# Performance work log

Measured on AMD Instinct MI355X. Metric: run time of the kernel, lower is better.

Reference implementation:

```python
import jax, jax.numpy as jnp
import numpy as np

FS = 11        # filter_size
N_ITER = 5     # mean-field iterations


def _unfold(x, fs):
    """x: (B, C, Hp, Wp) padded -> patches (B, C, H, W, fs, fs) with
    patches[b,c,h,w,i,j] == x[b,c,h+i,w+j]."""
    B, C, Hp, Wp = x.shape
    H, W = Hp - fs + 1, Wp - fs + 1
    p = jax.lax.conv_general_dilated_patches(
        x.reshape(B * C, 1, Hp, Wp), (fs, fs), (1, 1), 'VALID')  # (B*C, fs*fs, H, W)
    return p.reshape(B, C, fs, fs, H, W).transpose(0, 1, 4, 5, 2, 3)


def _smoothing_filter(fs, inv_bw, spacings):
    """Gaussian spatial filter with zeroed center, shape (B, fs, fs)."""
    r = jnp.arange(-(fs // 2), fs // 2 + 1, dtype=spacings.dtype)
    d = jnp.stack(jnp.meshgrid(r, r, indexing='ij'))           # (2, fs, fs)
    d = d[None] * spacings[:, :, None, None]                   # (B, 2, fs, fs)
    f = jnp.exp(-jnp.sum((d * inv_bw) ** 2 / 2, axis=1))       # (B, fs, fs)
    return f.at[:, fs // 2, fs // 2].set(0.0)


def setup_inputs() -> dict:
    key = jax.random.key(0)
    k1, k2 = jax.random.split(key)
    B, C, CH, H, W = 2, 6, 3, 192, 192
    return {
        'x': jax.random.normal(k1, (B, C, H, W), dtype=jnp.float32),
        'features': jax.random.normal(k2, (B, CH, H, W), dtype=jnp.float32),
        'spatial_spacings': jnp.ones((B, 2), dtype=jnp.float32),
        'smoothing_weight': jnp.array(1.0, dtype=jnp.float32),
        'appearance_weight': jnp.array(1.0, dtype=jnp.float32),
        'inverse_smoothing_bandwidth': jnp.array(1.0, dtype=jnp.float32),
        'inverse_appearance_bandwidth': jnp.array(1.0, dtype=jnp.float32),
    }


def reference(x, features, spatial_spacings, smoothing_weight, appearance_weight,
              inverse_smoothing_bandwidth, inverse_appearance_bandwidth):
    fs, pad = FS, FS // 2
    B, C, H, W = x.shape
    pad_cfg = [(0, 0), (0, 0), (pad, pad), (pad, pad)]

    # Spatial Gaussian filter (iteration-independent).
    sf = _smoothing_filter(fs, inverse_smoothing_bandwidth, spatial_spacings)  # (B,fs,fs)

    # Bilateral (appearance) filter, also iteration-independent -> hoisted.
    fpatch = _unfold(jnp.pad(features, pad_cfg), fs)           # (B,ch,H,W,fs,fs)
    diffs = features[..., None, None] - fpatch
    af = jnp.exp(-jnp.sum((diffs * inverse_appearance_bandwidth) ** 2 / 2, axis=1))  # (B,H,W,fs,fs)
    af = af.at[..., fs // 2, fs // 2].set(0.0)

    # combined message filter: w_s * sf + w_a * sf * af  (center tap already zero)
    sfb = sf[:, None, None]                                    # (B,1,1,fs,fs)
    total_filter = smoothing_weight * jnp.broadcast_to(sfb, af.shape) + appearance_weight * sfb * af

    compat = -jnp.eye(C, dtype=x.dtype)                        # Potts compatibility mu(l,l') = -[l==l']
    negative_unary = x
    for _ in range(N_ITER):
        q = jax.nn.softmax(x, axis=1)
        qpatch = _unfold(jnp.pad(q, pad_cfg), fs)              # (B,C,H,W,fs,fs)
        msg = jnp.einsum('bhwij,bchwij->bchw', total_filter, qpatch)
        x = negative_unary - jnp.einsum('bjhw,jk->bkhw', msg, compat)
    return jax.nn.log_softmax(x, axis=1)
```

## Files before the change

kernel.cpp:

```cpp
#include <hip/hip_runtime.h>

#define HH 192
#define WW 192
#define BB 2
#define NC 6
#define NF 3
#define FSZ 11
#define PAD 5
#define TW 16
#define TH 8
#define SWD (TW + 2*PAD)
#define SHT (TH + 2*PAD)
#define LQ 33
#define LF 33
#define HW (HH*WW)
#define NW 8
#define BT (NW*64)

template<bool FIRST, bool LAST>
__global__ __launch_bounds__(BT)
void crf_iter(const float* __restrict__ qsrc, const float* __restrict__ xun,
              const float* __restrict__ feats, const float* __restrict__ spac,
              const float* __restrict__ swp, const float* __restrict__ awp,
              const float* __restrict__ isbp, const float* __restrict__ iabp,
              float* __restrict__ dst)
{
    __shared__ float2 qp[3][SHT][LQ];
    __shared__ float4 ff[SHT][LF];
    __shared__ float  sfw[FSZ*FSZ];
    __shared__ float  sfa[FSZ*FSZ];
    __shared__ float  pm[NW][12][65];

    const int tid = threadIdx.x;
    const int b  = blockIdx.z;
    const int w0 = blockIdx.x * TW;
    const int h0 = blockIdx.y * TH;

    const float sw  = swp[0];
    const float aw  = awp[0];
    const float isb = isbp[0];
    const float iab = iabp[0];
    const float s0  = spac[b*2 + 0];
    const float s1  = spac[b*2 + 1];
    const float kapp = -0.5f * iab * iab;

    for (int t = tid; t < FSZ*FSZ; t += BT) {
        const int fi = t / FSZ;
        const int fj = t - fi*FSZ;
        const float ri = (float)(fi - PAD) * s0 * isb;
        const float rj = (float)(fj - PAD) * s1 * isb;
        float sf = __expf(-0.5f * (ri*ri + rj*rj));
        if (fi == PAD && fj == PAD) sf = 0.0f;
        sfw[t] = sf * sw;
        sfa[t] = sf * aw;
    }

    const float* fb = feats + (size_t)b * NF * HW;

    for (int idx = tid; idx < SHT*SWD; idx += BT) {
        const int sr = idx / SWD;
        const int sc = idx - sr*SWD;
        const int gh = h0 + sr - PAD;
        const int gw = w0 + sc - PAD;
        float q0=0.f,q1=0.f,q2=0.f,q3=0.f,q4=0.f,q5=0.f,g0=0.f,g1=0.f,g2=0.f;
        if (gh >= 0 && gh < HH && gw >= 0 && gw < WW) {
            const int off = gh*WW + gw;
            if (FIRST) {
                const float* xb = qsrc + (size_t)b * NC * HW;
                const float v0 = xb[off];
                const float v1 = xb[off +   HW];
                const float v2 = xb[off + 2*HW];
                const float v3 = xb[off + 3*HW];
                const float v4 = xb[off + 4*HW];
                const float v5 = xb[off + 5*HW];
                float m = fmaxf(fmaxf(fmaxf(v0,v1),fmaxf(v2,v3)),fmaxf(v4,v5));
                q0 = __expf(v0-m); q1 = __expf(v1-m); q2 = __expf(v2-m);
                q3 = __expf(v3-m); q4 = __expf(v4-m); q5 = __expf(v5-m);
                const float rs = 1.0f / (q0+q1+q2+q3+q4+q5);
                q0*=rs; q1*=rs; q2*=rs; q3*=rs; q4*=rs; q5*=rs;
            } else {
                const float2* qpx = (const float2*)(qsrc + ((size_t)(b*HH + gh)*WW + gw)*NC);
                const float2 a01 = qpx[0];
                const float2 a23 = qpx[1];
                const float2 a45 = qpx[2];
                q0=a01.x; q1=a01.y; q2=a23.x; q3=a23.y; q4=a45.x; q5=a45.y;
            }
            g0 = fb[off]; g1 = fb[off+HW]; g2 = fb[off+2*HW];
        }
        qp[0][sr][sc] = make_float2(q0,q1);
        qp[1][sr][sc] = make_float2(q2,q3);
        qp[2][sr][sc] = make_float2(q4,q5);
        ff[sr][sc]    = make_float4(g0,g1,g2,0.f);
    }

    const int g   = tid >> 6;
    const int t64 = tid & 63;
    const int tx  = t64 & 7;
    const int ty  = t64 >> 3;
    const int lr  = ty;
    const int lc0 = tx*2;

    __syncthreads();

    const float4 fa = ff[lr+PAD][lc0+PAD];
    const float4 fbx= ff[lr+PAD][lc0+PAD+1];

    float msgA[NC], msgB[NC];
    #pragma unroll
    for (int c = 0; c < NC; ++c) { msgA[c]=0.f; msgB[c]=0.f; }

    #pragma unroll 1
    for (int ir = 0; ir < 2; ++ir) {
        const int i = g + 8*ir;
        if (i >= FSZ) break;
        const int r = lr + i;
        const float* srw = &sfw[i*FSZ];
        const float* sra = &sfa[i*FSZ];
        #pragma unroll
        for (int a = 0; a < FSZ+1; ++a) {
            const int cc = lc0 + a;
            const float2 q01 = qp[0][r][cc];
            const float2 q23 = qp[1][r][cc];
            const float2 q45 = qp[2][r][cc];
            const float4 gv  = ff[r][cc];
            if (a < FSZ) {
                const float d0 = fa.x-gv.x, d1 = fa.y-gv.y, d2 = fa.z-gv.z;
                const float t  = fmaf(d2,d2, fmaf(d1,d1, d0*d0));
                const float af = __expf(t * kapp);
                const float tf = fmaf(af, sra[a], srw[a]);
                msgA[0] = fmaf(tf, q01.x, msgA[0]);
                msgA[1] = fmaf(tf, q01.y, msgA[1]);
                msgA[2] = fmaf(tf, q23.x, msgA[2]);
                msgA[3] = fmaf(tf, q23.y, msgA[3]);
                msgA[4] = fmaf(tf, q45.x, msgA[4]);
                msgA[5] = fmaf(tf, q45.y, msgA[5]);
            }
            if (a >= 1) {
                const float d0 = fbx.x-gv.x, d1 = fbx.y-gv.y, d2 = fbx.z-gv.z;
                const float t  = fmaf(d2,d2, fmaf(d1,d1, d0*d0));
                const float af = __expf(t * kapp);
                const float tf = fmaf(af, sra[a-1], srw[a-1]);
                msgB[0] = fmaf(tf, q01.x, msgB[0]);
                msgB[1] = fmaf(tf, q01.y, msgB[1]);
                msgB[2] = fmaf(tf, q23.x, msgB[2]);
                msgB[3] = fmaf(tf, q23.y, msgB[3]);
                msgB[4] = fmaf(tf, q45.x, msgB[4]);
                msgB[5] = fmaf(tf, q45.y, msgB[5]);
            }
        }
    }

    #pragma unroll
    for (int c = 0; c < NC; ++c) {
        pm[g][c][t64]   = msgA[c];
        pm[g][6+c][t64] = msgB[c];
    }
    __syncthreads();

    if (tid < 128) {
        const int pair  = tid >> 1;
        const int which = tid & 1;
        float xn[NC];
        #pragma unroll
        for (int c = 0; c < NC; ++c) {
            float s = 0.f;
            #pragma unroll
            for (int gr = 0; gr < NW; ++gr) s += pm[gr][which*6+c][pair];
            xn[c] = s;
        }
        const int gh = h0 + (pair >> 3);
        const int gw = w0 + ((pair & 7) * 2) + which;
        const size_t pbase = (size_t)b * NC * HW + (size_t)gh * WW + gw;
        const float* up = xun + pbase;
        #pragma unroll
        for (int c = 0; c < NC; ++c) xn[c] += up[(size_t)c*HW];

        float m = xn[0];
        #pragma unroll
        for (int c = 1; c < NC; ++c) m = fmaxf(m, xn[c]);

        if (LAST) {
            float s = 0.f;
            #pragma unroll
            for (int c = 0; c < NC; ++c) s += __expf(xn[c]-m);
            const float l = m + __logf(s);
            float* dp = dst + pbase;
            #pragma unroll
            for (int c = 0; c < NC; ++c) dp[(size_t)c*HW] = xn[c] - l;
        } else {
            float e[NC];
            float s = 0.f;
            #pragma unroll
            for (int c = 0; c < NC; ++c) { e[c] = __expf(xn[c]-m); s += e[c]; }
            const float rs = 1.0f / s;
            float2* qpx = (float2*)(dst + ((size_t)(b*HH + gh)*WW + gw)*NC);
            qpx[0] = make_float2(e[0]*rs, e[1]*rs);
            qpx[1] = make_float2(e[2]*rs, e[3]*rs);
            qpx[2] = make_float2(e[4]*rs, e[5]*rs);
        }
    }
}

extern "C" void kernel_launch(void* const* d_in, const int* in_sizes, int n_in,
                              void* d_out, int out_size, void* d_ws, size_t ws_size,
                              hipStream_t stream)
{
    const float* x    = (const float*)d_in[0];
    const float* fts  = (const float*)d_in[1];
    const float* spc  = (const float*)d_in[2];
    const float* swp  = (const float*)d_in[3];
    const float* awp  = (const float*)d_in[4];
    const float* isbp = (const float*)d_in[5];
    const float* iabp = (const float*)d_in[6];
    float* out = (float*)d_out;
    float* ws0 = (float*)d_ws;
    float* ws1 = (float*)d_ws + (size_t)NC*HW*BB;

    dim3 grid(WW/TW, HH/TH, BB);
    dim3 blk(BT);

    crf_iter<true ,false><<<grid, blk, 0, stream>>>(x,   x, fts, spc, swp, awp, isbp, iabp, ws0);
    crf_iter<false,false><<<grid, blk, 0, stream>>>(ws0, x, fts, spc, swp, awp, isbp, iabp, ws1);
    crf_iter<false,false><<<grid, blk, 0, stream>>>(ws1, x, fts, spc, swp, awp, isbp, iabp, ws0);
    crf_iter<false,false><<<grid, blk, 0, stream>>>(ws0, x, fts, spc, swp, awp, isbp, iabp, ws1);
    crf_iter<false,true ><<<grid, blk, 0, stream>>>(ws1, x, fts, spc, swp, awp, isbp, iabp, out);
}
```

Baseline: 62.39 us.

## Pack q and features into bf16 uint4 records and retile to four pixels per lane

Stores the softmax probabilities and the first two scaled features as packed bf16 in a single 16-byte record per pixel, with the third feature kept as a separate fp32 plane. Later iterations load this packed layout instead of fp32 planes. The inner loop is restructured so each lane computes four horizontally adjacent outputs over half of a filter row, and the two halves are reduced with a cross-lane shuffle. The aim is to cut LDS and global traffic and raise data reuse per lane. In exchange, q and features lose precision through bf16 rounding, and the register count per lane rises.

After: 64.34 us. 3.1% more time.

```diff
diff --git a/kernel.cpp b/kernel.cpp
--- a/kernel.cpp
+++ b/kernel.cpp
@@ -4,176 +4,206 @@
 #define WW 192
 #define BB 2
 #define NC 6
-#define NF 3
 #define FSZ 11
 #define PAD 5
 #define TW 16
 #define TH 8
-#define SWD (TW + 2*PAD)
-#define SHT (TH + 2*PAD)
-#define LQ 33
-#define LF 33
+#define SWD 26
+#define SHT 18
+#define LA 33
 #define HW (HH*WW)
-#define NW 8
-#define BT (NW*64)
+#define BT 512
+
+__device__ __forceinline__ unsigned pkbf(float a, float b) {
+    unsigned ua = (__float_as_uint(a) + 0x8000u) >> 16;
+    unsigned ub = (__float_as_uint(b) + 0x8000u) & 0xffff0000u;
+    return ua | ub;
+}
+__device__ __forceinline__ float lo16(unsigned u){ return __uint_as_float(u << 16); }
+__device__ __forceinline__ float hi16(unsigned u){ return __uint_as_float(u & 0xffff0000u); }
 
 template<bool FIRST, bool LAST>
-__global__ __launch_bounds__(BT)
-void crf_iter(const float* __restrict__ qsrc, const float* __restrict__ xun,
-              const float* __restrict__ feats, const float* __restrict__ spac,
-              const float* __restrict__ swp, const float* __restrict__ awp,
-              const float* __restrict__ isbp, const float* __restrict__ iabp,
-              float* __restrict__ dst)
+__global__ __launch_bounds__(BT, 4)
+void crf_iter(const float* __restrict__ xpl, const uint4* __restrict__ Ain,
+              const float* __restrict__ f2in, const float* __restrict__ feats,
+              const float* __restrict__ spac, const float* __restrict__ swp,
+              const float* __restrict__ awp, const float* __restrict__ isbp,
+              const float* __restrict__ iabp,
+              uint4* __restrict__ Aout, float* __restrict__ f2out,
+              float* __restrict__ outp)
 {
-    __shared__ float2 qp[3][SHT][LQ];
-    __shared__ float4 ff[SHT][LF];
-    __shared__ float  sfw[FSZ*FSZ];
-    __shared__ float  sfa[FSZ*FSZ];
-    __shared__ float  pm[NW][12][65];
+    __shared__ uint4 A[SHT][LA];
+    __shared__ float F2[SHT][LA];
+    __shared__ float sfw[FSZ*FSZ];
+    __shared__ float sfa[FSZ*FSZ];
+    __shared__ float pm[8][NC][132];
 
     const int tid = threadIdx.x;
     const int b  = blockIdx.z;
     const int w0 = blockIdx.x * TW;
     const int h0 = blockIdx.y * TH;
 
-    const float sw  = swp[0];
-    const float aw  = awp[0];
-    const float isb = isbp[0];
-    const float iab = iabp[0];
-    const float s0  = spac[b*2 + 0];
-    const float s1  = spac[b*2 + 1];
-    const float kapp = -0.5f * iab * iab;
-
-    for (int t = tid; t < FSZ*FSZ; t += BT) {
-        const int fi = t / FSZ;
-        const int fj = t - fi*FSZ;
-        const float ri = (float)(fi - PAD) * s0 * isb;
-        const float rj = (float)(fj - PAD) * s1 * isb;
-        float sf = __expf(-0.5f * (ri*ri + rj*rj));
-        if (fi == PAD && fj == PAD) sf = 0.0f;
-        sfw[t] = sf * sw;
-        sfa[t] = sf * aw;
-    }
-
-    const float* fb = feats + (size_t)b * NF * HW;
+    const float swv = swp[0], awv = awp[0], isb = isbp[0], iab = iabp[0];
+    const float s0 = spac[b*2], s1 = spac[b*2+1];
+    const float sfac = iab * 0.70710678f;
+
+    if (tid < FSZ*FSZ) {
+        const int fi = tid / FSZ, fj = tid - (tid/FSZ)*FSZ;
+        const float ri = (float)(fi-PAD) * s0 * isb;
+        const float rj = (float)(fj-PAD) * s1 * isb;
+        float sf = __expf(-0.5f*(ri*ri + rj*rj));
+        if (fi == PAD && fj == PAD) sf = 0.f;
+        sfw[tid] = sf * swv;
+        sfa[tid] = sf * awv;
+    }
 
     for (int idx = tid; idx < SHT*SWD; idx += BT) {
-        const int sr = idx / SWD;
-        const int sc = idx - sr*SWD;
-        const int gh = h0 + sr - PAD;
-        const int gw = w0 + sc - PAD;
-        float q0=0.f,q1=0.f,q2=0.f,q3=0.f,q4=0.f,q5=0.f,g0=0.f,g1=0.f,g2=0.f;
+        const int sr = idx / SWD, sc = idx - (idx/SWD)*SWD;
+        const int gh = h0 + sr - PAD, gw = w0 + sc - PAD;
+        uint4 av = make_uint4(0u,0u,0u,0u);
+        float f2v = 0.f;
         if (gh >= 0 && gh < HH && gw >= 0 && gw < WW) {
-            const int off = gh*WW + gw;
             if (FIRST) {
-                const float* xb = qsrc + (size_t)b * NC * HW;
-                const float v0 = xb[off];
-                const float v1 = xb[off +   HW];
-                const float v2 = xb[off + 2*HW];
-                const float v3 = xb[off + 3*HW];
-                const float v4 = xb[off + 4*HW];
-                const float v5 = xb[off + 5*HW];
+                const int off = gh*WW + gw;
+                const float* xb = xpl + (size_t)b*NC*HW + off;
+                const float v0 = xb[0];
+                const float v1 = xb[HW];
+                const float v2 = xb[2*HW];
+                const float v3 = xb[3*HW];
+                const float v4 = xb[4*HW];
+                const float v5 = xb[5*HW];
                 float m = fmaxf(fmaxf(fmaxf(v0,v1),fmaxf(v2,v3)),fmaxf(v4,v5));
-                q0 = __expf(v0-m); q1 = __expf(v1-m); q2 = __expf(v2-m);
-                q3 = __expf(v3-m); q4 = __expf(v4-m); q5 = __expf(v5-m);
-                const float rs = 1.0f / (q0+q1+q2+q3+q4+q5);
+                float q0=__expf(v0-m), q1=__expf(v1-m), q2=__expf(v2-m);
+                float q3=__expf(v3-m), q4=__expf(v4-m), q5=__expf(v5-m);
+                const float rs = 1.0f/(q0+q1+q2+q3+q4+q5);
                 q0*=rs; q1*=rs; q2*=rs; q3*=rs; q4*=rs; q5*=rs;
+                const float* fb = feats + (size_t)b*3*HW + off;
+                const float g0 = fb[0]*sfac, g1 = fb[HW]*sfac, g2 = fb[2*HW]*sfac;
+                av = make_uint4(pkbf(q0,q1), pkbf(q2,q3), pkbf(q4,q5), pkbf(g0,g1));
+                f2v = g2;
             } else {
-                const float2* qpx = (const float2*)(qsrc + ((size_t)(b*HH + gh)*WW + gw)*NC);
-                const float2 a01 = qpx[0];
-                const float2 a23 = qpx[1];
-                const float2 a45 = qpx[2];
-                q0=a01.x; q1=a01.y; q2=a23.x; q3=a23.y; q4=a45.x; q5=a45.y;
+                const size_t p = (size_t)(b*HH + gh)*WW + gw;
+                av  = Ain[p];
+                f2v = f2in[p];
             }
-            g0 = fb[off]; g1 = fb[off+HW]; g2 = fb[off+2*HW];
-        }
-        qp[0][sr][sc] = make_float2(q0,q1);
-        qp[1][sr][sc] = make_float2(q2,q3);
-        qp[2][sr][sc] = make_float2(q4,q5);
-        ff[sr][sc]    = make_float4(g0,g1,g2,0.f);
-    }
-
-    const int g   = tid >> 6;
-    const int t64 = tid & 63;
-    const int tx  = t64 & 7;
-    const int ty  = t64 >> 3;
-    const int lr  = ty;
-    const int lc0 = tx*2;
+        }
+        A[sr][sc]  = av;
+        F2[sr][sc] = f2v;
+    }
+
+    const int w    = tid >> 6;
+    const int l    = tid & 63;
+    const int half = l >> 5;
+    const int lh   = l & 31;
+    const int ry   = lh >> 2;
+    const int lc0  = (lh & 3) * 4;
+    const int jb   = half * 6;
 
     __syncthreads();
 
-    const float4 fa = ff[lr+PAD][lc0+PAD];
-    const float4 fbx= ff[lr+PAD][lc0+PAD+1];
-
-    float msgA[NC], msgB[NC];
+    float cf0[4], cf1[4], cf2[4];
     #pragma unroll
-    for (int c = 0; c < NC; ++c) { msgA[c]=0.f; msgB[c]=0.f; }
-
-    #pragma unroll 1
-    for (int ir = 0; ir < 2; ++ir) {
-        const int i = g + 8*ir;
-        if (i >= FSZ) break;
-        const int r = lr + i;
-        const float* srw = &sfw[i*FSZ];
-        const float* sra = &sfa[i*FSZ];
-        #pragma unroll
-        for (int a = 0; a < FSZ+1; ++a) {
-            const int cc = lc0 + a;
-            const float2 q01 = qp[0][r][cc];
-            const float2 q23 = qp[1][r][cc];
-            const float2 q45 = qp[2][r][cc];
-            const float4 gv  = ff[r][cc];
-            if (a < FSZ) {
-                const float d0 = fa.x-gv.x, d1 = fa.y-gv.y, d2 = fa.z-gv.z;
+    for (int k = 0; k < 4; ++k) {
+        const unsigned fw = A[ry+PAD][lc0+PAD+k].w;
+        cf0[k] = lo16(fw);
+        cf1[k] = hi16(fw);
+        cf2[k] = F2[ry+PAD][lc0+PAD+k];
+    }
+
+    float msg[4][NC];
+    #pragma unroll
+    for (int k = 0; k < 4; ++k)
+        #pragma unroll
+        for (int c = 0; c < NC; ++c) msg[k][c] = 0.f;
+
+    auto row_pass = [&](int i) {
+        const int r = ry + i;
+        const uint4* Ar = &A[r][lc0 + jb];
+        const float* Fr = &F2[r][lc0 + jb];
+        float srwR[6], sraR[6];
+        #pragma unroll
+        for (int d = 0; d < 6; ++d) {
+            const int jj = jb + d;
+            const bool v = (jj < FSZ);
+            srwR[d] = v ? sfw[i*FSZ + jj] : 0.f;
+            sraR[d] = v ? sfa[i*FSZ + jj] : 0.f;
+        }
+        #pragma unroll
+        for (int a = 0; a < 8; ++a) {
+            const uint4 av = Ar[a];
+            const float g2 = Fr[a];
+            const float q0 = lo16(av.x), q1 = hi16(av.x);
+            const float q2 = lo16(av.y), q3 = hi16(av.y);
+            const float q4 = lo16(av.z), q5 = hi16(av.z);
+            const float g0 = lo16(av.w), g1 = hi16(av.w);
+            #pragma unroll
+            for (int k = 0; k < 4; ++k) {
+                const int d = a - k;
+                if (d < 0 || d > 5) continue;
+                const float d0 = cf0[k]-g0, d1 = cf1[k]-g1, d2 = cf2[k]-g2;
                 const float t  = fmaf(d2,d2, fmaf(d1,d1, d0*d0));
-                const float af = __expf(t * kapp);
-                const float tf = fmaf(af, sra[a], srw[a]);
-                msgA[0] = fmaf(tf, q01.x, msgA[0]);
-                msgA[1] = fmaf(tf, q01.y, msgA[1]);
-                msgA[2] = fmaf(tf, q23.x, msgA[2]);
-                msgA[3] = fmaf(tf, q23.y, msgA[3]);
-                msgA[4] = fmaf(tf, q45.x, msgA[4]);
-                msgA[5] = fmaf(tf, q45.y, msgA[5]);
+                const float af = __expf(-t);
+                const float tf = fmaf(af, sraR[d], srwR[d]);
+                msg[k][0] = fmaf(tf,q0,msg[k][0]);
+                msg[k][1] = fmaf(tf,q1,msg[k][1]);
+                msg[k][2] = fmaf(tf,q2,msg[k][2]);
+                msg[k][3] = fmaf(tf,q3,msg[k][3]);
+                msg[k][4] = fmaf(tf,q4,msg[k][4]);
+                msg[k][5] = fmaf(tf,q5,msg[k][5]);
             }
-            if (a >= 1) {
-                const float d0 = fbx.x-gv.x, d1 = fbx.y-gv.y, d2 = fbx.z-gv.z;
-                const float t  = fmaf(d2,d2, fmaf(d1,d1, d0*d0));
-                const float af = __expf(t * kapp);
-                const float tf = fmaf(af, sra[a-1], srw[a-1]);
-                msgB[0] = fmaf(tf, q01.x, msgB[0]);
-                msgB[1] = fmaf(tf, q01.y, msgB[1]);
-                msgB[2] = fmaf(tf, q23.x, msgB[2]);
-                msgB[3] = fmaf(tf, q23.y, msgB[3]);
-                msgB[4] = fmaf(tf, q45.x, msgB[4]);
-                msgB[5] = fmaf(tf, q45.y, msgB[5]);
-            }
-        }
-    }
+        }
+        if (jb == 0) {
+            const uint4 av = Ar[8];
+            const float g2 = Fr[8];
+            const float q0 = lo16(av.x), q1 = hi16(av.x);
+            const float q2 = lo16(av.y), q3 = hi16(av.y);
+            const float q4 = lo16(av.z), q5 = hi16(av.z);
+            const float g0 = lo16(av.w), g1 = hi16(av.w);
+            const float d0 = cf0[3]-g0, d1 = cf1[3]-g1, d2 = cf2[3]-g2;
+            const float t  = fmaf(d2,d2, fmaf(d1,d1, d0*d0));
+            const float af = __expf(-t);
+            const float tf = fmaf(af, sraR[5], srwR[5]);
+            msg[3][0] = fmaf(tf,q0,msg[3][0]);
+            msg[3][1] = fmaf(tf,q1,msg[3][1]);
+            msg[3][2] = fmaf(tf,q2,msg[3][2]);
+            msg[3][3] = fmaf(tf,q3,msg[3][3]);
+            msg[3][4] = fmaf(tf,q4,msg[3][4]);
+            msg[3][5] = fmaf(tf,q5,msg[3][5]);
+        }
+    };
+
+    row_pass(w);
+    if (w < 3) row_pass(w + 8);
 
     #pragma unroll
-    for (int c = 0; c < NC; ++c) {
-        pm[g][c][t64]   = msgA[c];
-        pm[g][6+c][t64] = msgB[c];
+    for (int k = 0; k < 4; ++k)
+        #pragma unroll
+        for (int c = 0; c < NC; ++c)
+            msg[k][c] += __shfl_xor(msg[k][c], 32);
+
+    if (half == 0) {
+        #pragma unroll
+        for (int c = 0; c < NC; ++c) {
+            float4 v = make_float4(msg[0][c], msg[1][c], msg[2][c], msg[3][c]);
+            *(float4*)&pm[w][c][ry*16 + lc0] = v;
+        }
     }
     __syncthreads();
 
-    if (tid < 128) {
-        const int pair  = tid >> 1;
-        const int which = tid & 1;
+    if (tid < TW*TH) {
+        const int col = tid & 15, rw = tid >> 4;
         float xn[NC];
         #pragma unroll
         for (int c = 0; c < NC; ++c) {
             float s = 0.f;
             #pragma unroll
-            for (int gr = 0; gr < NW; ++gr) s += pm[gr][which*6+c][pair];
+            for (int g = 0; g < 8; ++g) s += pm[g][c][tid];
             xn[c] = s;
         }
-        const int gh = h0 + (pair >> 3);
-        const int gw = w0 + ((pair & 7) * 2) + which;
-        const size_t pbase = (size_t)b * NC * HW + (size_t)gh * WW + gw;
-        const float* up = xun + pbase;
-        #pragma unroll
-        for (int c = 0; c < NC; ++c) xn[c] += up[(size_t)c*HW];
+        const int gh = h0 + rw, gw = w0 + col;
+        const size_t pb = (size_t)b*NC*HW + (size_t)gh*WW + gw;
+        #pragma unroll
+        for (int c = 0; c < NC; ++c) xn[c] += xpl[pb + (size_t)c*HW];
 
         float m = xn[0];
         #pragma unroll
@@ -183,20 +213,20 @@
             float s = 0.f;
             #pragma unroll
             for (int c = 0; c < NC; ++c) s += __expf(xn[c]-m);
-            const float l = m + __logf(s);
-            float* dp = dst + pbase;
-            #pragma unroll
-            for (int c = 0; c < NC; ++c) dp[(size_t)c*HW] = xn[c] - l;
+            const float lg = m + __logf(s);
+            #pragma unroll
+            for (int c = 0; c < NC; ++c) outp[pb + (size_t)c*HW] = xn[c] - lg;
         } else {
-            float e[NC];
-            float s = 0.f;
+            float e[NC]; float s = 0.f;
             #pragma unroll
             for (int c = 0; c < NC; ++c) { e[c] = __expf(xn[c]-m); s += e[c]; }
             const float rs = 1.0f / s;
-            float2* qpx = (float2*)(dst + ((size_t)(b*HH + gh)*WW + gw)*NC);
-            qpx[0] = make_float2(e[0]*rs, e[1]*rs);
-            qpx[1] = make_float2(e[2]*rs, e[3]*rs);
-            qpx[2] = make_float2(e[4]*rs, e[5]*rs);
+            const unsigned f01 = A[rw+PAD][col+PAD].w;
+            const size_t p = (size_t)(b*HH + gh)*WW + gw;
+            Aout[p] = make_uint4(pkbf(e[0]*rs, e[1]*rs),
+                                 pkbf(e[2]*rs, e[3]*rs),
+                                 pkbf(e[4]*rs, e[5]*rs), f01);
+            if (FIRST) f2out[p] = F2[rw+PAD][col+PAD];
         }
     }
 }
@@ -213,15 +243,17 @@
     const float* isbp = (const float*)d_in[5];
     const float* iabp = (const float*)d_in[6];
     float* out = (float*)d_out;
-    float* ws0 = (float*)d_ws;
-    float* ws1 = (float*)d_ws + (size_t)NC*HW*BB;
+
+    uint4* A0  = (uint4*)d_ws;
+    uint4* A1  = A0 + (size_t)BB*HW;
+    float* f2s = (float*)(A1 + (size_t)BB*HW);
 
     dim3 grid(WW/TW, HH/TH, BB);
     dim3 blk(BT);
 
-    crf_iter<true ,false><<<grid, blk, 0, stream>>>(x,   x, fts, spc, swp, awp, isbp, iabp, ws0);
-    crf_iter<false,false><<<grid, blk, 0, stream>>>(ws0, x, fts, spc, swp, awp, isbp, iabp, ws1);
-    crf_iter<false,false><<<grid, blk, 0, stream>>>(ws1, x, fts, spc, swp, awp, isbp, iabp, ws0);
-    crf_iter<false,false><<<grid, blk, 0, stream>>>(ws0, x, fts, spc, swp, awp, isbp, iabp, ws1);
-    crf_iter<false,true ><<<grid, blk, 0, stream>>>(ws1, x, fts, spc, swp, awp, isbp, iabp, out);
+    crf_iter<true ,false><<<grid, blk, 0, stream>>>(x, A1, f2s, fts, spc, swp, awp, isbp, iabp, A0, f2s, out);
+    crf_iter<false,false><<<grid, blk, 0, stream>>>(x, A0, f2s, fts, spc, swp, awp, isbp, iabp, A1, f2s, out);
+    crf_iter<false,false><<<grid, blk, 0, stream>>>(x, A1, f2s, fts, spc, swp, awp, isbp, iabp, A0, f2s, out);
+    crf_iter<false,false><<<grid, blk, 0, stream>>>(x, A0, f2s, fts, spc, swp, awp, isbp, iabp, A1, f2s, out);
+    crf_iter<false,true ><<<grid, blk, 0, stream>>>(x, A1, f2s, fts, spc, swp, awp, isbp, iabp, A0, f2s, out);
 }
```
